# Kernel optimization log

Measured on AMD Instinct MI355X. Metric: run time of the kernel, lower is better.

The kernel has to match this reference:

```python
import jax, jax.numpy as jnp
import numpy as np

HID = 3584; NH = 16; NKV = 8; HD = 256; S = 3072; WIN = 2048
SOFTCAP = 50.0; QSCALE = 256.0 ** -0.5  # query_pre_attn_scalar = 256
NEG = -2.3819763e38


def _rope(x, cos, sin):
    # x: (B, S, heads, HD); cos/sin: (S, HD//2). Gemma half-split complex RoPE.
    x1, x2 = jnp.split(x, 2, axis=-1)
    c = cos[None, :, None, :]
    s = sin[None, :, None, :]
    return jnp.concatenate([x1 * c - x2 * s, x1 * s + x2 * c], axis=-1)


def setup_inputs() -> dict:
    key = jax.random.key(0)
    k1, k2, k3 = jax.random.split(key, 3)
    hidden_states = jax.random.normal(k1, (1, S, HID), jnp.float32)
    qkv_w = jax.random.normal(k2, (NH * HD + 2 * NKV * HD, HID), jnp.float32) * 0.02
    o_w = jax.random.normal(k3, (HID, NH * HD), jnp.float32) * 0.02
    inv = 1.0 / (10000.0 ** (jnp.arange(0, HD, 2, dtype=jnp.float32) / HD))
    ang = jnp.arange(S, dtype=jnp.float32)[:, None] * inv[None, :]
    freqs_cis = jnp.stack([jnp.cos(ang), jnp.sin(ang)], axis=-1)  # (S, HD//2, 2)
    kv_write_indices = jnp.arange(S, dtype=jnp.int32)
    k_cache = jnp.zeros((1, S, NKV, HD), jnp.float32)
    v_cache = jnp.zeros((1, S, NKV, HD), jnp.float32)
    i = jnp.arange(S)[:, None]
    j = jnp.arange(S)[None, :]
    mask = jnp.where(j <= i, 0.0, NEG).astype(jnp.float32)[None, None]  # causal (1,1,S,S)
    return dict(hidden_states=hidden_states, freqs_cis=freqs_cis,
                kv_write_indices=kv_write_indices, k_cache=k_cache, v_cache=v_cache,
                mask=mask, qkv_w=qkv_w, o_w=o_w)


def reference(hidden_states, freqs_cis, kv_write_indices, k_cache, v_cache, mask, qkv_w, o_w):
    B, L, _ = hidden_states.shape
    qkv = hidden_states @ qkv_w.T  # (B, L, 8192)
    xq, xk, xv = jnp.split(qkv, [NH * HD, NH * HD + NKV * HD], axis=-1)
    xq = xq.reshape(B, L, NH, HD)
    xk = xk.reshape(B, L, NKV, HD)
    xv = xv.reshape(B, L, NKV, HD)
    cos, sin = freqs_cis[..., 0], freqs_cis[..., 1]
    xq = _rope(xq, cos, sin)
    xk = _rope(xk, cos, sin)
    # KV cache index_copy_ on dim 1
    k_all = k_cache.at[:, kv_write_indices].set(xk)  # (B, T, NKV, HD)
    v_all = v_cache.at[:, kv_write_indices].set(xv)
    T = k_all.shape[1]
    G = NH // NKV  # queries per kv head; grouped einsum avoids repeat_interleave
    q = (xq * QSCALE).transpose(0, 2, 1, 3).reshape(B, NKV, G, L, HD)
    k = k_all.transpose(0, 2, 1, 3)  # (B, NKV, T, HD)
    v = v_all.transpose(0, 2, 1, 3)
    scores = jnp.einsum('bkgsd,bktd->bkgst', q, k)
    # logit softcapping
    scores = jnp.tanh(scores / SOFTCAP) * SOFTCAP
    # sliding-window band applied on top of the provided (causal) mask
    i = jnp.arange(L)[:, None]
    j = jnp.arange(T)[None, :]
    band = (j >= i - WIN + 1) & (j <= i + WIN - 1)
    m = jnp.where(band, mask, NEG)  # (1,1,L,T)
    scores = scores + m[:, :, None]  # broadcast over group dim
    probs = jax.nn.softmax(scores.astype(jnp.float32), axis=-1).astype(q.dtype)
    out = jnp.einsum('bkgst,bktd->bkgsd', probs, v)
    out = out.reshape(B, NH, L, HD).transpose(0, 2, 1, 3).reshape(B, L, NH * HD)
    return out @ o_w.T
```

## Files before the change

### kernel.cpp

```cpp
#include <hip/hip_runtime.h>

#define S_LEN 3072
#define NHQ 16
#define NKVH 8
#define HDIM 256
#define WIN 2048
#define QKV_COLS 8192

typedef __bf16 bf16x8 __attribute__((ext_vector_type(8)));
typedef float f32x4 __attribute__((ext_vector_type(4)));
typedef float f32x16 __attribute__((ext_vector_type(16)));

__device__ __forceinline__ unsigned short f2bf(float f) {
    union { float f; unsigned u; } v; v.f = f;
    unsigned r = v.u + 0x7FFFu + ((v.u >> 16) & 1u);
    return (unsigned short)(r >> 16);
}
__device__ __forceinline__ float bf2f(unsigned short u) {
    union { unsigned u; float f; } v; v.u = ((unsigned)u) << 16; return v.f;
}

typedef __attribute__((address_space(3))) void lds_void_t;
typedef const __attribute__((address_space(1))) void glb_void_t;
__device__ __forceinline__ void async16(const void* g, void* l) {
    __builtin_amdgcn_global_load_lds((glb_void_t*)g, (lds_void_t*)l, 16, 0, 0);
}

__global__ __launch_bounds__(256) void cast_bf16_kernel(const float* __restrict__ src,
                                                        unsigned short* __restrict__ dst,
                                                        int n) {
    int i = (blockIdx.x * 256 + threadIdx.x) * 4;
    if (i >= n) return;
    float4 v = *(const float4*)(src + i);
    ushort4 o;
    o.x = f2bf(v.x); o.y = f2bf(v.y); o.z = f2bf(v.z); o.w = f2bf(v.w);
    *(ushort4*)(dst + i) = o;
}

template <int OUT_BF16>
__global__ __launch_bounds__(256) void gemm_bt(const unsigned short* __restrict__ A,
                                               const unsigned short* __restrict__ B,
                                               void* __restrict__ Cv,
                                               int N, int K) {
    __shared__ __align__(16) unsigned short At[128 * 32];
    __shared__ __align__(16) unsigned short Bt[128 * 32];
    const int tid = threadIdx.x;
    const int wid = tid >> 6, lane = tid & 63;
    const int ln = lane & 15, quad = lane >> 4;

    int bm, bn;
    {
        const int nwg = gridDim.x * gridDim.y;
        int orig = blockIdx.y * gridDim.x + blockIdx.x;
        int wg = orig;
        if ((nwg & 7) == 0) {
            const int cpx = nwg >> 3;
            wg = (orig & 7) * cpx + (orig >> 3);
        }
        bm = wg / gridDim.x;
        bn = wg % gridDim.x;
    }
    const int wm = wid >> 1, wn = wid & 1;

    const f32x4 fzero = {0.f, 0.f, 0.f, 0.f};
    f32x4 acc[4][4];
#pragma unroll
    for (int i = 0; i < 4; i++) {
#pragma unroll
        for (int j = 0; j < 4; j++) acc[i][j] = fzero;
    }

    const unsigned short* gA = A + (size_t)(bm * 128 + wid * 32 + (lane >> 2)) * K + (lane & 3) * 8;
    const unsigned short* gB = B + (size_t)(bn * 128 + wid * 32 + (lane >> 2)) * K + (lane & 3) * 8;
    unsigned short* lA = At + wid * 32 * 32;
    unsigned short* lB = Bt + wid * 32 * 32;

    for (int k0 = 0; k0 < K; k0 += 32) {
        async16(gA + k0, lA);
        async16(gA + k0 + 16 * K, lA + 16 * 32);
        async16(gB + k0, lB);
        async16(gB + k0 + 16 * K, lB + 16 * 32);
        __syncthreads();

        bf16x8 af[4], bfr[4];
#pragma unroll
        for (int mt = 0; mt < 4; mt++)
            af[mt] = *(const bf16x8*)(At + (wm * 64 + mt * 16 + ln) * 32 + quad * 8);
#pragma unroll
        for (int nt = 0; nt < 4; nt++)
            bfr[nt] = *(const bf16x8*)(Bt + (wn * 64 + nt * 16 + ln) * 32 + quad * 8);
#pragma unroll
        for (int mt = 0; mt < 4; mt++) {
#pragma unroll
            for (int nt = 0; nt < 4; nt++)
                acc[mt][nt] = __builtin_amdgcn_mfma_f32_16x16x32_bf16(af[mt], bfr[nt], acc[mt][nt], 0, 0, 0);
        }
        __syncthreads();
    }

    const int row0 = bm * 128 + wm * 64 + quad * 4;
    const int col0 = bn * 128 + wn * 64 + ln;
    if (OUT_BF16) {
        unsigned short* C = (unsigned short*)Cv;
#pragma unroll
        for (int mt = 0; mt < 4; mt++) {
#pragma unroll
            for (int nt = 0; nt < 4; nt++) {
#pragma unroll
                for (int rr = 0; rr < 4; rr++)
                    C[(size_t)(row0 + mt * 16 + rr) * N + col0 + nt * 16] = f2bf(acc[mt][nt][rr]);
            }
        }
    } else {
        float* C = (float*)Cv;
#pragma unroll
        for (int mt = 0; mt < 4; mt++) {
#pragma unroll
            for (int nt = 0; nt < 4; nt++) {
#pragma unroll
                for (int rr = 0; rr < 4; rr++)
                    C[(size_t)(row0 + mt * 16 + rr) * N + col0 + nt * 16] = acc[mt][nt][rr];
            }
        }
    }
}

__global__ __launch_bounds__(256) void rope_kernel(const unsigned short* __restrict__ qkv,
                                                   const float* __restrict__ freqs,
                                                   const int* __restrict__ kvidx,
                                                   unsigned short* __restrict__ Qb,
                                                   unsigned short* __restrict__ Kb) {
    int t = blockIdx.x * 256 + threadIdx.x;
    int d = t & 127;
    int t2 = t >> 7;
    int hh = t2 % 24;
    int pos = t2 / 24;
    if (pos >= S_LEN) return;
    float2 cs = *(const float2*)(freqs + ((size_t)pos * 128 + d) * 2);
    if (hh < NHQ) {
        const unsigned short* src = qkv + (size_t)pos * QKV_COLS + hh * HDIM + d;
        float x1 = bf2f(src[0]), x2 = bf2f(src[128]);
        float o1 = (x1 * cs.x - x2 * cs.y) * 0.0625f;
        float o2 = (x1 * cs.y + x2 * cs.x) * 0.0625f;
        unsigned short* dst = Qb + ((size_t)hh * S_LEN + pos) * HDIM + d;
        dst[0] = f2bf(o1);
        dst[128] = f2bf(o2);
    } else {
        int kvh = hh - NHQ;
        const unsigned short* src = qkv + (size_t)pos * QKV_COLS + NHQ * HDIM + kvh * HDIM + d;
        float x1 = bf2f(src[0]), x2 = bf2f(src[128]);
        float o1 = x1 * cs.x - x2 * cs.y;
        float o2 = x1 * cs.y + x2 * cs.x;
        int wpos = kvidx[pos];
        unsigned short* dst = Kb + ((size_t)kvh * S_LEN + wpos) * HDIM + d;
        dst[0] = f2bf(o1);
        dst[128] = f2bf(o2);
    }
}

__global__ __launch_bounds__(256) void vtrans_kernel(const unsigned short* __restrict__ qkv,
                                                     const int* __restrict__ kvidx,
                                                     unsigned short* __restrict__ Vbt) {
    __shared__ unsigned short T[64][72];
    int pos0 = blockIdx.x * 64;
    int c0 = blockIdx.y * 64;
    int a = threadIdx.x >> 6;
    int b = threadIdx.x & 63;
#pragma unroll
    for (int r = 0; r < 16; r++) {
        int pl = r * 4 + a;
        T[pl][b] = qkv[(size_t)(pos0 + pl) * QKV_COLS + 6144 + c0 + b];
    }
    __syncthreads();
    int wpos = kvidx[pos0 + b];
#pragma unroll
    for (int r = 0; r < 16; r++) {
        int cl = r * 4 + a;
        Vbt[(size_t)(c0 + cl) * S_LEN + wpos] = T[b][cl];
    }
}

__global__ __launch_bounds__(256, 1) void attn_kernel(const unsigned short* __restrict__ Qb,
                                                      const unsigned short* __restrict__ Kb,
                                                      const unsigned short* __restrict__ Vbt,
                                                      float* __restrict__ Acc,
                                                      float* __restrict__ Ps,
                                                      unsigned short* __restrict__ attn_out) {
    __shared__ __align__(16) unsigned short Kl[2][32 * 256];
    __shared__ __align__(16) unsigned short Vl[2][256 * 32];
    __shared__ __align__(16) unsigned short Plb[4][1024];

    const int h = blockIdx.x / 80;
    const int it = 79 - (blockIdx.x % 80);
    int qb, sub, nc;
    if (it < 4)       { qb = it; sub = 0; nc = 1; }
    else if (it < 12) { int e = it - 4;  qb = 4 + (e >> 1); sub = e & 1;  nc = 2; }
    else if (it < 24) { int e = it - 12; qb = 8 + e / 3;    sub = e % 3;  nc = 3; }
    else if (it < 40) { int e = it - 24; qb = 12 + (e >> 2); sub = e & 3; nc = 4; }
    else              { int e = it - 40; qb = 16 + e / 5;   sub = e % 5;  nc = 5; }

    const int kv = h >> 1;
    const int q0 = qb * 128;
    const int tid = threadIdx.x;
    const int wid = tid >> 6, lane = tid & 63;
    const int ln32 = lane & 31, hi = lane >> 5;
    const int qw0 = q0 + wid * 32;

    bf16x8 qf[16];
    {
        const unsigned short* qrow = Qb + ((size_t)h * S_LEN + qw0 + ln32) * HDIM + hi * 8;
#pragma unroll
        for (int s = 0; s < 16; s++)
            qf[s] = *(const bf16x8*)(qrow + s * 16);
    }

    f32x16 pacc[8];
#pragma unroll
    for (int dt = 0; dt < 8; dt++) {
#pragma unroll
        for (int i = 0; i < 16; i++) pacc[dt][i] = 0.f;
    }
    float ps[16];
#pragma unroll
    for (int r = 0; r < 16; r++) ps[r] = 0.f;

    const int imin = qw0;
    const int imax = qw0 + 31;

    const int t_lo = (q0 >= WIN) ? ((q0 - (WIN - 1)) >> 5) : 0;
    const int t_hi = (q0 + 127) >> 5;
    const int tn = t_hi - t_lo + 1;
    const int ts = t_lo + (tn * sub) / nc;
    const int te = t_lo + (tn * (sub + 1)) / nc;

    const unsigned short* kSrcA = Kb + ((size_t)kv * S_LEN + (tid >> 5)) * HDIM
                                  + ((tid & 31) ^ ((tid >> 5) & 7)) * 8;
    const unsigned short* vSrcA = Vbt + ((size_t)kv * HDIM + (tid >> 2)) * S_LEN
                                  + ((tid & 3) ^ ((tid >> 3) & 3)) * 8;

    {
        const int p0s = ts * 32;
        const unsigned short* ksg = kSrcA + (size_t)p0s * HDIM;
        const unsigned short* vsg = vSrcA + p0s;
#pragma unroll
        for (int c = 0; c < 4; c++)
            async16(ksg + (size_t)(c * 8) * HDIM, &Kl[0][(c * 256 + tid) * 8]);
#pragma unroll
        for (int c = 0; c < 4; c++)
            async16(vsg + (size_t)(c * 64) * S_LEN, &Vl[0][(c * 256 + tid) * 8]);
    }

    unsigned short* plw = &Plb[wid][0];
    const int kswz = ln32 & 7;
    int cur = 0;

    for (int tt = ts; tt < te; tt++) {
        asm volatile("s_waitcnt vmcnt(0)" ::: "memory");
        __builtin_amdgcn_s_barrier();
        asm volatile("" ::: "memory");

        if (tt + 1 < te) {
            const int p0n = (tt + 1) * 32;
            const unsigned short* ksg = kSrcA + (size_t)p0n * HDIM;
            const unsigned short* vsg = vSrcA + p0n;
#pragma unroll
            for (int c = 0; c < 4; c++)
                async16(ksg + (size_t)(c * 8) * HDIM, &Kl[cur ^ 1][(c * 256 + tid) * 8]);
#pragma unroll
            for (int c = 0; c < 4; c++)
                async16(vsg + (size_t)(c * 64) * S_LEN, &Vl[cur ^ 1][(c * 256 + tid) * 8]);
        }

        const int p0 = tt * 32;
        const bool live = (p0 <= imax) && (p0 + 31 >= imin - WIN + 1);
        if (live) {
            const unsigned short* kb = Kl[cur];
            f32x16 sacc;
#pragma unroll
            for (int i = 0; i < 16; i++) sacc[i] = 0.f;
#pragma unroll
            for (int s = 0; s < 16; s++) {
                bf16x8 kf = *(const bf16x8*)(kb + ln32 * 256 + ((((s << 1) + hi) ^ kswz) << 3));
                sacc = __builtin_amdgcn_mfma_f32_32x32x16_bf16(qf[s], kf, sacc, 0, 0, 0);
            }

            const bool full = (p0 + 31 <= imin) && (p0 >= imax - WIN + 1);
#pragma unroll
            for (int r = 0; r < 16; r++) {
                float z = __expf(sacc[r] * 0.04f);
                float t = fmaf(-100.f, __builtin_amdgcn_rcpf(z + 1.f), 50.f);
                float p = __expf(t);
                const int qloc = (r & 3) + 8 * (r >> 2) + 4 * hi;
                if (!full) {
                    const int i = qw0 + qloc;
                    const int j = p0 + ln32;
                    p = ((j <= i) && (j + WIN > i)) ? p : 0.f;
                }
                ps[r] += p;
                plw[qloc * 32 + (((ln32 >> 3) ^ ((qloc >> 1) & 3)) << 3) + (ln32 & 7)] = f2bf(p);
            }

            bf16x8 pa0 = *(const bf16x8*)(plw + ln32 * 32 + ((hi ^ ((ln32 >> 1) & 3)) << 3));
            bf16x8 pa1 = *(const bf16x8*)(plw + ln32 * 32 + (((2 + hi) ^ ((ln32 >> 1) & 3)) << 3));
            const unsigned short* vb = Vl[cur];
#pragma unroll
            for (int dt = 0; dt < 8; dt++) {
                const int d = dt * 32 + ln32;
                const int vswz = (d >> 1) & 3;
                bf16x8 v0 = *(const bf16x8*)(vb + d * 32 + ((hi ^ vswz) << 3));
                pacc[dt] = __builtin_amdgcn_mfma_f32_32x32x16_bf16(pa0, v0, pacc[dt], 0, 0, 0);
                bf16x8 v1 = *(const bf16x8*)(vb + d * 32 + (((2 + hi) ^ vswz) << 3));
                pacc[dt] = __builtin_amdgcn_mfma_f32_32x32x16_bf16(pa1, v1, pacc[dt], 0, 0, 0);
            }
        }
        cur ^= 1;
    }

#pragma unroll
    for (int r = 0; r < 16; r++) {
        float s = ps[r];
#pragma unroll
        for (int o = 1; o <= 16; o <<= 1)
            s += __shfl_xor(s, o);
        ps[r] = s;
    }

    if (nc == 1) {
#pragma unroll
        for (int dt = 0; dt < 8; dt++) {
#pragma unroll
            for (int r = 0; r < 16; r++) {
                const int q = qw0 + (r & 3) + 8 * (r >> 2) + 4 * hi;
                float o = pacc[dt][r] * __builtin_amdgcn_rcpf(ps[r]);
                attn_out[(size_t)q * 4096 + h * HDIM + dt * 32 + ln32] = f2bf(o);
            }
        }
    } else {
        if (ln32 == 0) {
#pragma unroll
            for (int r = 0; r < 16; r++) {
                const int q = qw0 + (r & 3) + 8 * (r >> 2) + 4 * hi;
                atomicAdd(&Ps[h * S_LEN + q], ps[r]);
            }
        }
#pragma unroll
        for (int dt = 0; dt < 8; dt++) {
#pragma unroll
            for (int r = 0; r < 16; r++) {
                const int q = qw0 + (r & 3) + 8 * (r >> 2) + 4 * hi;
                atomicAdd(&Acc[((size_t)h * S_LEN + q) * HDIM + dt * 32 + ln32], pacc[dt][r]);
            }
        }
    }
}

__global__ __launch_bounds__(256) void norm_kernel(const float* __restrict__ Acc,
                                                   const float* __restrict__ Ps,
                                                   unsigned short* __restrict__ attn_out) {
    int row = blockIdx.x * 4 + (threadIdx.x >> 6);
    int lane = threadIdx.x & 63;
    int h = row / 2560;
    int pos = 512 + (row - h * 2560);
    float4 a = *(const float4*)(Acc + ((size_t)h * S_LEN + pos) * HDIM + lane * 4);
    float inv = __builtin_amdgcn_rcpf(Ps[h * S_LEN + pos]);
    ushort4 o;
    o.x = f2bf(a.x * inv); o.y = f2bf(a.y * inv);
    o.z = f2bf(a.z * inv); o.w = f2bf(a.w * inv);
    *(ushort4*)(attn_out + (size_t)pos * 4096 + h * HDIM + lane * 4) = o;
}

extern "C" void kernel_launch(void* const* d_in, const int* in_sizes, int n_in,
                              void* d_out, int out_size, void* d_ws, size_t ws_size,
                              hipStream_t stream) {
    (void)in_sizes; (void)n_in; (void)out_size; (void)ws_size;
    const float* hidden = (const float*)d_in[0];
    const float* freqs  = (const float*)d_in[1];
    const int* kvidx    = (const int*)d_in[2];
    const float* qkv_w  = (const float*)d_in[6];
    const float* o_w    = (const float*)d_in[7];
    float* out = (float*)d_out;

    char* ws = (char*)d_ws;
    unsigned short* hs_bf   = (unsigned short*)(ws);
    unsigned short* w1_bf   = (unsigned short*)(ws + 22020096);
    unsigned short* w2_bf   = (unsigned short*)(ws + 80740352);
    unsigned short* qkv_bf  = (unsigned short*)(ws + 110100480);
    unsigned short* Qb      = (unsigned short*)(ws + 160432128);
    unsigned short* Kb      = (unsigned short*)(ws + 185597952);
    unsigned short* Vbt     = (unsigned short*)(ws + 198180864);
    unsigned short* attn_bf = (unsigned short*)(ws + 210763776);

    float* Acc = (float*)(ws + 110100480);
    float* Ps  = (float*)(ws);

    cast_bf16_kernel<<<10752, 256, 0, stream>>>(hidden, hs_bf, 11010048);
    cast_bf16_kernel<<<28672, 256, 0, stream>>>(qkv_w, w1_bf, 29360128);
    cast_bf16_kernel<<<14336, 256, 0, stream>>>(o_w, w2_bf, 14680064);

    gemm_bt<1><<<dim3(64, 24), 256, 0, stream>>>(hs_bf, w1_bf, (void*)qkv_bf, 8192, 3584);

    rope_kernel<<<36864, 256, 0, stream>>>(qkv_bf, freqs, kvidx, Qb, Kb);
    vtrans_kernel<<<dim3(48, 32), 256, 0, stream>>>(qkv_bf, kvidx, Vbt);

    hipMemsetAsync(Acc, 0, (size_t)16 * 3072 * 256 * 4, stream);
    hipMemsetAsync(Ps, 0, (size_t)16 * 3072 * 4, stream);

    attn_kernel<<<1280, 256, 0, stream>>>(Qb, Kb, Vbt, Acc, Ps, attn_bf);
    norm_kernel<<<10240, 256, 0, stream>>>(Acc, Ps, attn_bf);

    gemm_bt<0><<<dim3(28, 24), 256, 0, stream>>>(attn_bf, w2_bf, (void*)out, 3584, 4096);
}
```

Measured before the change: 1.014 ms.

## Drop split-KV atomics; one block per head and query tile with triple buffering

The attention kernel no longer splits each query block's key range across several workgroups. Each of the 384 blocks now handles the whole key range for one head and 128-query tile, normalises in registers and writes bf16 output directly. This removes the Acc/Ps memsets, the fp32 atomic accumulation traffic and the separate normalisation kernel. K/V staging also goes from double to triple buffering with a partial vmcnt wait, so loads are issued two tiles ahead. The cost is a coarser grid with uneven per-block work (the longest blocks walk 68 key tiles), which relies on the heaviest-first block ordering for load balance, plus more LDS per block.

```diff
diff --git a/kernel.cpp b/kernel.cpp
--- a/kernel.cpp
+++ b/kernel.cpp
@@ -183,21 +183,13 @@
 __global__ __launch_bounds__(256, 1) void attn_kernel(const unsigned short* __restrict__ Qb,
                                                       const unsigned short* __restrict__ Kb,
                                                       const unsigned short* __restrict__ Vbt,
-                                                      float* __restrict__ Acc,
-                                                      float* __restrict__ Ps,
                                                       unsigned short* __restrict__ attn_out) {
-    __shared__ __align__(16) unsigned short Kl[2][32 * 256];
-    __shared__ __align__(16) unsigned short Vl[2][256 * 32];
+    __shared__ __align__(16) unsigned short Kl[3][32 * 256];
+    __shared__ __align__(16) unsigned short Vl[3][256 * 32];
     __shared__ __align__(16) unsigned short Plb[4][1024];
 
-    const int h = blockIdx.x / 80;
-    const int it = 79 - (blockIdx.x % 80);
-    int qb, sub, nc;
-    if (it < 4)       { qb = it; sub = 0; nc = 1; }
-    else if (it < 12) { int e = it - 4;  qb = 4 + (e >> 1); sub = e & 1;  nc = 2; }
-    else if (it < 24) { int e = it - 12; qb = 8 + e / 3;    sub = e % 3;  nc = 3; }
-    else if (it < 40) { int e = it - 24; qb = 12 + (e >> 2); sub = e & 3; nc = 4; }
-    else              { int e = it - 40; qb = 16 + e / 5;   sub = e % 5;  nc = 5; }
+    const int h = blockIdx.x & 15;
+    const int qb = 23 - (blockIdx.x >> 4);
 
     const int kv = h >> 1;
     const int q0 = qb * 128;
@@ -229,52 +221,48 @@
 
     const int t_lo = (q0 >= WIN) ? ((q0 - (WIN - 1)) >> 5) : 0;
     const int t_hi = (q0 + 127) >> 5;
-    const int tn = t_hi - t_lo + 1;
-    const int ts = t_lo + (tn * sub) / nc;
-    const int te = t_lo + (tn * (sub + 1)) / nc;
+    const int ts = t_lo;
+    const int te = t_hi + 1;
 
     const unsigned short* kSrcA = Kb + ((size_t)kv * S_LEN + (tid >> 5)) * HDIM
                                   + ((tid & 31) ^ ((tid >> 5) & 7)) * 8;
     const unsigned short* vSrcA = Vbt + ((size_t)kv * HDIM + (tid >> 2)) * S_LEN
                                   + ((tid & 3) ^ ((tid >> 3) & 3)) * 8;
 
-    {
-        const int p0s = ts * 32;
-        const unsigned short* ksg = kSrcA + (size_t)p0s * HDIM;
-        const unsigned short* vsg = vSrcA + p0s;
+    auto STAGE = [&](int tile, int b) {
+        const int p0x = tile * 32;
+        const unsigned short* ksg = kSrcA + (size_t)p0x * HDIM;
+        const unsigned short* vsg = vSrcA + p0x;
 #pragma unroll
         for (int c = 0; c < 4; c++)
-            async16(ksg + (size_t)(c * 8) * HDIM, &Kl[0][(c * 256 + tid) * 8]);
+            async16(ksg + (size_t)(c * 8) * HDIM, &Kl[b][(c * 256 + tid) * 8]);
 #pragma unroll
         for (int c = 0; c < 4; c++)
-            async16(vsg + (size_t)(c * 64) * S_LEN, &Vl[0][(c * 256 + tid) * 8]);
-    }
+            async16(vsg + (size_t)(c * 64) * S_LEN, &Vl[b][(c * 256 + tid) * 8]);
+    };
+
+    STAGE(ts, 0);
+    STAGE(ts + 1, 1);
 
     unsigned short* plw = &Plb[wid][0];
     const int kswz = ln32 & 7;
-    int cur = 0;
+    int rb = 0;
 
     for (int tt = ts; tt < te; tt++) {
-        asm volatile("s_waitcnt vmcnt(0)" ::: "memory");
+        if (tt + 1 < te) { asm volatile("s_waitcnt vmcnt(8)" ::: "memory"); }
+        else             { asm volatile("s_waitcnt vmcnt(0)" ::: "memory"); }
         __builtin_amdgcn_s_barrier();
         asm volatile("" ::: "memory");
 
-        if (tt + 1 < te) {
-            const int p0n = (tt + 1) * 32;
-            const unsigned short* ksg = kSrcA + (size_t)p0n * HDIM;
-            const unsigned short* vsg = vSrcA + p0n;
-#pragma unroll
-            for (int c = 0; c < 4; c++)
-                async16(ksg + (size_t)(c * 8) * HDIM, &Kl[cur ^ 1][(c * 256 + tid) * 8]);
-#pragma unroll
-            for (int c = 0; c < 4; c++)
-                async16(vsg + (size_t)(c * 64) * S_LEN, &Vl[cur ^ 1][(c * 256 + tid) * 8]);
+        if (tt + 2 < te) {
+            const int wb = (rb >= 1) ? rb - 1 : 2;
+            STAGE(tt + 2, wb);
         }
 
         const int p0 = tt * 32;
         const bool live = (p0 <= imax) && (p0 + 31 >= imin - WIN + 1);
         if (live) {
-            const unsigned short* kb = Kl[cur];
+            const unsigned short* kb = Kl[rb];
             f32x16 sacc;
 #pragma unroll
             for (int i = 0; i < 16; i++) sacc[i] = 0.f;
@@ -302,7 +290,7 @@
 
             bf16x8 pa0 = *(const bf16x8*)(plw + ln32 * 32 + ((hi ^ ((ln32 >> 1) & 3)) << 3));
             bf16x8 pa1 = *(const bf16x8*)(plw + ln32 * 32 + (((2 + hi) ^ ((ln32 >> 1) & 3)) << 3));
-            const unsigned short* vb = Vl[cur];
+            const unsigned short* vb = Vl[rb];
 #pragma unroll
             for (int dt = 0; dt < 8; dt++) {
                 const int d = dt * 32 + ln32;
@@ -313,7 +301,7 @@
                 pacc[dt] = __builtin_amdgcn_mfma_f32_32x32x16_bf16(pa1, v1, pacc[dt], 0, 0, 0);
             }
         }
-        cur ^= 1;
+        rb = (rb >= 2) ? 0 : rb + 1;
     }
 
 #pragma unroll
@@ -325,48 +313,15 @@
         ps[r] = s;
     }
 
-    if (nc == 1) {
-#pragma unroll
-        for (int dt = 0; dt < 8; dt++) {
-#pragma unroll
-            for (int r = 0; r < 16; r++) {
-                const int q = qw0 + (r & 3) + 8 * (r >> 2) + 4 * hi;
-                float o = pacc[dt][r] * __builtin_amdgcn_rcpf(ps[r]);
-                attn_out[(size_t)q * 4096 + h * HDIM + dt * 32 + ln32] = f2bf(o);
-            }
-        }
-    } else {
-        if (ln32 == 0) {
-#pragma unroll
-            for (int r = 0; r < 16; r++) {
-                const int q = qw0 + (r & 3) + 8 * (r >> 2) + 4 * hi;
-                atomicAdd(&Ps[h * S_LEN + q], ps[r]);
-            }
-        }
-#pragma unroll
-        for (int dt = 0; dt < 8; dt++) {
-#pragma unroll
-            for (int r = 0; r < 16; r++) {
-                const int q = qw0 + (r & 3) + 8 * (r >> 2) + 4 * hi;
-                atomicAdd(&Acc[((size_t)h * S_LEN + q) * HDIM + dt * 32 + ln32], pacc[dt][r]);
-            }
-        }
-    }
-}
-
-__global__ __launch_bounds__(256) void norm_kernel(const float* __restrict__ Acc,
-                                                   const float* __restrict__ Ps,
-                                                   unsigned short* __restrict__ attn_out) {
-    int row = blockIdx.x * 4 + (threadIdx.x >> 6);
-    int lane = threadIdx.x & 63;
-    int h = row / 2560;
-    int pos = 512 + (row - h * 2560);
-    float4 a = *(const float4*)(Acc + ((size_t)h * S_LEN + pos) * HDIM + lane * 4);
-    float inv = __builtin_amdgcn_rcpf(Ps[h * S_LEN + pos]);
-    ushort4 o;
-    o.x = f2bf(a.x * inv); o.y = f2bf(a.y * inv);
-    o.z = f2bf(a.z * inv); o.w = f2bf(a.w * inv);
-    *(ushort4*)(attn_out + (size_t)pos * 4096 + h * HDIM + lane * 4) = o;
+#pragma unroll
+    for (int dt = 0; dt < 8; dt++) {
+#pragma unroll
+        for (int r = 0; r < 16; r++) {
+            const int q = qw0 + (r & 3) + 8 * (r >> 2) + 4 * hi;
+            float o = pacc[dt][r] * __builtin_amdgcn_rcpf(ps[r]);
+            attn_out[(size_t)q * 4096 + h * HDIM + dt * 32 + ln32] = f2bf(o);
+        }
+    }
 }
 
 extern "C" void kernel_launch(void* const* d_in, const int* in_sizes, int n_in,
@@ -390,9 +345,6 @@
     unsigned short* Vbt     = (unsigned short*)(ws + 198180864);
     unsigned short* attn_bf = (unsigned short*)(ws + 210763776);
 
-    float* Acc = (float*)(ws + 110100480);
-    float* Ps  = (float*)(ws);
-
     cast_bf16_kernel<<<10752, 256, 0, stream>>>(hidden, hs_bf, 11010048);
     cast_bf16_kernel<<<28672, 256, 0, stream>>>(qkv_w, w1_bf, 29360128);
     cast_bf16_kernel<<<14336, 256, 0, stream>>>(o_w, w2_bf, 14680064);
@@ -402,11 +354,7 @@
     rope_kernel<<<36864, 256, 0, stream>>>(qkv_bf, freqs, kvidx, Qb, Kb);
     vtrans_kernel<<<dim3(48, 32), 256, 0, stream>>>(qkv_bf, kvidx, Vbt);
 
-    hipMemsetAsync(Acc, 0, (size_t)16 * 3072 * 256 * 4, stream);
-    hipMemsetAsync(Ps, 0, (size_t)16 * 3072 * 4, stream);
-
-    attn_kernel<<<1280, 256, 0, stream>>>(Qb, Kb, Vbt, Acc, Ps, attn_bf);
-    norm_kernel<<<10240, 256, 0, stream>>>(Acc, Ps, attn_bf);
+    attn_kernel<<<384, 256, 0, stream>>>(Qb, Kb, Vbt, attn_bf);
 
     gemm_bt<0><<<dim3(28, 24), 256, 0, stream>>>(attn_bf, w2_bf, (void*)out, 3584, 4096);
 }
```

After: 904.3 us. -10.8%, faster.
